# Performance work log

Measured on AMD Instinct MI355X. Metric: run time of the kernel, lower is better.

## Reference

```python
import jax, jax.numpy as jnp
import numpy as np

N = 8192
D = 512


def setup_inputs() -> dict:
    key = jax.random.key(0)
    k1, k2, k3, k4 = jax.random.split(key, 4)
    U = jax.random.normal(k1, (N, D), dtype=jnp.float32)
    V = jax.random.normal(k2, (N, D), dtype=jnp.float32)
    M = jax.random.normal(k3, (N, N), dtype=jnp.float32)
    W = jax.random.uniform(k4, (N, N), dtype=jnp.float32)
    alpha = jnp.ones((1,), dtype=jnp.float32) * 0.1
    return {"U": U, "V": V, "M": M, "W": W, "alpha": alpha}


def reference(U, V, M, W, alpha):
    # Reconstruction term: sum((U V^T - M)^2)
    recon = U @ V.T                                  # (N, N) GEMM
    part1 = jnp.sum(jnp.square(recon - M))
    # Manifold term in closed form:
    # sum_{i,j} W[i,j] * ||U_i - V_j||^2
    #   = sum_i rowW_i ||U_i||^2 + sum_j colW_j ||V_j||^2 - 2 sum(W * U V^T)
    u_sq = jnp.sum(U * U, axis=1)                    # (N,)
    v_sq = jnp.sum(V * V, axis=1)                    # (N,)
    row_w = jnp.sum(W, axis=1)                       # (N,)
    col_w = jnp.sum(W, axis=0)                       # (N,)
    cross = jnp.sum(W * recon)
    part2 = alpha[0] * (jnp.dot(row_w, u_sq) + jnp.dot(col_w, v_sq) - 2.0 * cross)
    total = part1 + part2
    return total / (M.shape[0] * M.shape[1])
```

## Files before the change

### kernel.cpp

```cpp
#include <hip/hip_runtime.h>
#include <hip/hip_bf16.h>
#include <stdint.h>

#define N_DIM 8192
#define D_DIM 512
#define BM 128
#define BN 128
#define BK 64

typedef __attribute__((ext_vector_type(8))) short bf16x8;
typedef __attribute__((ext_vector_type(4))) float f32x4;

__device__ __forceinline__ unsigned short f2bf(float f) {
    unsigned int x = __float_as_uint(f);
    x += 0x7fffu + ((x >> 16) & 1u);
    return (unsigned short)(x >> 16);
}

__global__ void __launch_bounds__(256) prep_kernel(
    const float* __restrict__ U, const float* __restrict__ V,
    unsigned short* __restrict__ Ub, unsigned short* __restrict__ Vb,
    float* __restrict__ usq, float* __restrict__ vsq)
{
    int row = blockIdx.x;
    const float* src;
    unsigned short* dst;
    float* sq;
    if (row < N_DIM) {
        src = U + (size_t)row * D_DIM;
        dst = Ub + (size_t)row * D_DIM;
        sq  = usq + row;
    } else {
        int r = row - N_DIM;
        src = V + (size_t)r * D_DIM;
        dst = Vb + (size_t)r * D_DIM;
        sq  = vsq + r;
    }
    int t = threadIdx.x;
    float2 v = *reinterpret_cast<const float2*>(src + 2 * t);
    float s = v.x * v.x + v.y * v.y;
    ushort2 b;
    b.x = f2bf(v.x);
    b.y = f2bf(v.y);
    *reinterpret_cast<ushort2*>(dst + 2 * t) = b;

    #pragma unroll
    for (int o = 32; o > 0; o >>= 1) s += __shfl_down(s, o, 64);
    __shared__ float red[4];
    if ((t & 63) == 0) red[t >> 6] = s;
    __syncthreads();
    if (t == 0) *sq = red[0] + red[1] + red[2] + red[3];
}

__global__ void __launch_bounds__(256, 4) fused_kernel(
    const unsigned short* __restrict__ Ub, const unsigned short* __restrict__ Vb,
    const float* __restrict__ Mg, const float* __restrict__ Wg,
    const float* __restrict__ usq, const float* __restrict__ vsq,
    double* __restrict__ acc)
{
    __shared__ alignas(16) char smem[BM * BK * 2 + BN * BK * 2];
    __shared__ float red1[4], red2[4];
    char* As = smem;
    char* Bs = smem + BM * BK * 2;
    float* recs = (float*)smem;

    const int t    = threadIdx.x;
    const int lane = t & 63;
    const int wave = t >> 6;
    const int wm   = wave >> 1;
    const int wn   = wave & 1;

    const int bid    = (blockIdx.x & 7) * 512 + (blockIdx.x >> 3);
    const int tile_m = bid >> 6;
    const int tile_n = bid & 63;
    const int row0   = tile_m * BM;
    const int col0   = tile_n * BN;

    const f32x4 zero = {0.f, 0.f, 0.f, 0.f};
    f32x4 acc_r[4][4];
    #pragma unroll
    for (int i = 0; i < 4; ++i)
        #pragma unroll
        for (int j = 0; j < 4; ++j)
            acc_r[i][j] = zero;

    auto As3 = (__attribute__((address_space(3))) char*)As;
    auto Bs3 = (__attribute__((address_space(3))) char*)Bs;

    for (int kt = 0; kt < D_DIM / BK; ++kt) {
        const int k0 = kt * BK;
        #pragma unroll
        for (int c = 0; c < 4; ++c) {
            int s   = c * 256 + t;
            int row = s >> 3;
            int kg  = s & 7;
            int kgs = kg ^ (row & 7);
            const unsigned short* ga = Ub + (size_t)(row0 + row) * D_DIM + k0 + kgs * 8;
            __builtin_amdgcn_global_load_lds(
                (const __attribute__((address_space(1))) void*)ga,
                (__attribute__((address_space(3))) void*)(As3 + s * 16), 16, 0, 0);
            const unsigned short* gb = Vb + (size_t)(col0 + row) * D_DIM + k0 + kgs * 8;
            __builtin_amdgcn_global_load_lds(
                (const __attribute__((address_space(1))) void*)gb,
                (__attribute__((address_space(3))) void*)(Bs3 + s * 16), 16, 0, 0);
        }
        __syncthreads();

        #pragma unroll
        for (int kc = 0; kc < 2; ++kc) {
            bf16x8 af[4], bfr[4];
            const int kgw = kc * 4 + (lane >> 4);
            #pragma unroll
            for (int i = 0; i < 4; ++i) {
                int ra   = wm * 64 + i * 16 + (lane & 15);
                int offa = ra * (BK * 2) + ((kgw ^ (ra & 7)) * 16);
                af[i] = *reinterpret_cast<const bf16x8*>(As + offa);
                int rb   = wn * 64 + i * 16 + (lane & 15);
                int offb = rb * (BK * 2) + ((kgw ^ (rb & 7)) * 16);
                bfr[i] = *reinterpret_cast<const bf16x8*>(Bs + offb);
            }
            #pragma unroll
            for (int i = 0; i < 4; ++i)
                #pragma unroll
                for (int j = 0; j < 4; ++j)
                    acc_r[i][j] = __builtin_amdgcn_mfma_f32_16x16x32_bf16(
                        af[i], bfr[j], acc_r[i][j], 0, 0, 0);
        }
        __syncthreads();
    }

    const int rloc = t >> 5;
    const int c4   = (t & 31) * 4;
    const f32x4 vs = *reinterpret_cast<const f32x4*>(vsq + col0 + c4);

    float s1 = 0.f, s2 = 0.f;

    #pragma unroll
    for (int h = 0; h < 2; ++h) {
        if (wm == h) {
            #pragma unroll
            for (int i = 0; i < 4; ++i)
                #pragma unroll
                for (int j = 0; j < 4; ++j)
                    #pragma unroll
                    for (int q = 0; q < 4; ++q)
                        recs[(i * 16 + (lane >> 4) * 4 + q) * 128 +
                             wn * 64 + j * 16 + (lane & 15)] = acc_r[i][j][q];
        }
        __syncthreads();

        const float* Mrow = Mg + (size_t)(row0 + h * 64) * N_DIM + col0 + c4;
        const float* Wrow = Wg + (size_t)(row0 + h * 64) * N_DIM + col0 + c4;

        #pragma unroll
        for (int kk = 0; kk < 2; ++kk) {
            f32x4 mv[4], wv[4];
            float usr[4];
            #pragma unroll
            for (int b = 0; b < 4; ++b) {
                int r = rloc + (kk * 4 + b) * 8;
                mv[b]  = *reinterpret_cast<const f32x4*>(Mrow + (size_t)r * N_DIM);
                wv[b]  = *reinterpret_cast<const f32x4*>(Wrow + (size_t)r * N_DIM);
                usr[b] = usq[row0 + h * 64 + r];
            }
            #pragma unroll
            for (int b = 0; b < 4; ++b) {
                int r = rloc + (kk * 4 + b) * 8;
                f32x4 rc = *reinterpret_cast<const f32x4*>(recs + r * 128 + c4);
                #pragma unroll
                for (int c = 0; c < 4; ++c) {
                    float d = rc[c] - mv[b][c];
                    s1 = fmaf(d, d, s1);
                    s2 = fmaf(wv[b][c], usr[b] + vs[c] - 2.f * rc[c], s2);
                }
            }
        }
        __syncthreads();
    }

    #pragma unroll
    for (int o = 32; o > 0; o >>= 1) {
        s1 += __shfl_down(s1, o, 64);
        s2 += __shfl_down(s2, o, 64);
    }
    if (lane == 0) { red1[wave] = s1; red2[wave] = s2; }
    __syncthreads();
    if (t == 0) {
        double a1 = (double)red1[0] + red1[1] + red1[2] + red1[3];
        double a2 = (double)red2[0] + red2[1] + red2[2] + red2[3];
        atomicAdd(acc, a1);
        atomicAdd(acc + 1, a2);
    }
}

__global__ void finalize_kernel(const double* __restrict__ acc,
                                const float* __restrict__ alpha,
                                float* __restrict__ out)
{
    double tot = acc[0] + (double)alpha[0] * acc[1];
    out[0] = (float)(tot / ((double)N_DIM * (double)N_DIM));
}

extern "C" void kernel_launch(void* const* d_in, const int* in_sizes, int n_in,
                              void* d_out, int out_size, void* d_ws, size_t ws_size,
                              hipStream_t stream) {
    const float* U     = (const float*)d_in[0];
    const float* V     = (const float*)d_in[1];
    const float* Mg    = (const float*)d_in[2];
    const float* Wg    = (const float*)d_in[3];
    const float* alpha = (const float*)d_in[4];

    char* ws = (char*)d_ws;
    unsigned short* Ub = (unsigned short*)ws;
    unsigned short* Vb = (unsigned short*)(ws + 8u * 1024 * 1024);
    float* usq = (float*)(ws + 16u * 1024 * 1024);
    float* vsq = (float*)(ws + 16u * 1024 * 1024 + 32u * 1024);
    double* acc = (double*)(ws + 16u * 1024 * 1024 + 64u * 1024);

    hipMemsetAsync(acc, 0, 2 * sizeof(double), stream);
    prep_kernel<<<2 * N_DIM, 256, 0, stream>>>(U, V, Ub, Vb, usq, vsq);
    fused_kernel<<<(N_DIM / BM) * (N_DIM / BN), 256, 0, stream>>>(
        Ub, Vb, Mg, Wg, usq, vsq, acc);
    finalize_kernel<<<1, 1, 0, stream>>>(acc, alpha, (float*)d_out);
}
```

Measured before the change: 202.4 us.

## Process two column tiles per block, overlapping epilogue with second GEMM

Each block now computes two adjacent 128x128 output tiles. The M/W epilogue of the first tile is interleaved into the MFMA k-loop of the second tile, so the streaming of the large M and W matrices overlaps with matrix-core work. The reconstruction tile moves into its own padded LDS buffer (stride 132) to reduce bank conflicts, and the swizzled block ordering is dropped. This doubles accumulator registers (launch bounds lowered to 2 blocks per SM) and halves the grid, which may reduce occupancy and latency hiding.

```diff
diff --git a/kernel.cpp b/kernel.cpp
--- a/kernel.cpp
+++ b/kernel.cpp
@@ -7,6 +7,7 @@
 #define BM 128
 #define BN 128
 #define BK 64
+#define RSTR 132
 
 typedef __attribute__((ext_vector_type(8))) short bf16x8;
 typedef __attribute__((ext_vector_type(4))) float f32x4;
@@ -52,17 +53,17 @@
     if (t == 0) *sq = red[0] + red[1] + red[2] + red[3];
 }
 
-__global__ void __launch_bounds__(256, 4) fused_kernel(
+__global__ void __launch_bounds__(256, 2) fused_kernel(
     const unsigned short* __restrict__ Ub, const unsigned short* __restrict__ Vb,
     const float* __restrict__ Mg, const float* __restrict__ Wg,
     const float* __restrict__ usq, const float* __restrict__ vsq,
     double* __restrict__ acc)
 {
     __shared__ alignas(16) char smem[BM * BK * 2 + BN * BK * 2];
+    __shared__ alignas(16) float recs[64 * RSTR];
     __shared__ float red1[4], red2[4];
     char* As = smem;
     char* Bs = smem + BM * BK * 2;
-    float* recs = (float*)smem;
 
     const int t    = threadIdx.x;
     const int lane = t & 63;
@@ -70,73 +71,58 @@
     const int wm   = wave >> 1;
     const int wn   = wave & 1;
 
-    const int bid    = (blockIdx.x & 7) * 512 + (blockIdx.x >> 3);
-    const int tile_m = bid >> 6;
-    const int tile_n = bid & 63;
+    const int bid    = blockIdx.x;
+    const int tile_m = bid >> 5;
+    const int pair   = bid & 31;
     const int row0   = tile_m * BM;
-    const int col0   = tile_n * BN;
-
-    const f32x4 zero = {0.f, 0.f, 0.f, 0.f};
-    f32x4 acc_r[4][4];
-    #pragma unroll
-    for (int i = 0; i < 4; ++i)
-        #pragma unroll
-        for (int j = 0; j < 4; ++j)
-            acc_r[i][j] = zero;
+    const int col0_0 = (pair * 2) * BN;
+    const int col0_1 = (pair * 2 + 1) * BN;
+
+    const int rloc = t >> 5;
+    const int c4   = (t & 31) * 4;
+
+    float s1 = 0.f, s2 = 0.f;
 
     auto As3 = (__attribute__((address_space(3))) char*)As;
     auto Bs3 = (__attribute__((address_space(3))) char*)Bs;
 
-    for (int kt = 0; kt < D_DIM / BK; ++kt) {
-        const int k0 = kt * BK;
+    auto stage = [&](const unsigned short* Ua, const unsigned short* Va, int k0) {
         #pragma unroll
         for (int c = 0; c < 4; ++c) {
             int s   = c * 256 + t;
             int row = s >> 3;
             int kg  = s & 7;
             int kgs = kg ^ (row & 7);
-            const unsigned short* ga = Ub + (size_t)(row0 + row) * D_DIM + k0 + kgs * 8;
             __builtin_amdgcn_global_load_lds(
-                (const __attribute__((address_space(1))) void*)ga,
+                (const __attribute__((address_space(1))) void*)(Ua + (size_t)row * D_DIM + k0 + kgs * 8),
                 (__attribute__((address_space(3))) void*)(As3 + s * 16), 16, 0, 0);
-            const unsigned short* gb = Vb + (size_t)(col0 + row) * D_DIM + k0 + kgs * 8;
             __builtin_amdgcn_global_load_lds(
-                (const __attribute__((address_space(1))) void*)gb,
+                (const __attribute__((address_space(1))) void*)(Va + (size_t)row * D_DIM + k0 + kgs * 8),
                 (__attribute__((address_space(3))) void*)(Bs3 + s * 16), 16, 0, 0);
         }
-        __syncthreads();
-
+    };
+
+    auto mma = [&](f32x4 (&a)[4][4]) {
         #pragma unroll
         for (int kc = 0; kc < 2; ++kc) {
             bf16x8 af[4], bfr[4];
             const int kgw = kc * 4 + (lane >> 4);
             #pragma unroll
             for (int i = 0; i < 4; ++i) {
-                int ra   = wm * 64 + i * 16 + (lane & 15);
-                int offa = ra * (BK * 2) + ((kgw ^ (ra & 7)) * 16);
-                af[i] = *reinterpret_cast<const bf16x8*>(As + offa);
-                int rb   = wn * 64 + i * 16 + (lane & 15);
-                int offb = rb * (BK * 2) + ((kgw ^ (rb & 7)) * 16);
-                bfr[i] = *reinterpret_cast<const bf16x8*>(Bs + offb);
+                int ra = wm * 64 + i * 16 + (lane & 15);
+                af[i]  = *reinterpret_cast<const bf16x8*>(As + ra * (BK * 2) + ((kgw ^ (ra & 7)) * 16));
+                int rb = wn * 64 + i * 16 + (lane & 15);
+                bfr[i] = *reinterpret_cast<const bf16x8*>(Bs + rb * (BK * 2) + ((kgw ^ (rb & 7)) * 16));
             }
             #pragma unroll
             for (int i = 0; i < 4; ++i)
                 #pragma unroll
                 for (int j = 0; j < 4; ++j)
-                    acc_r[i][j] = __builtin_amdgcn_mfma_f32_16x16x32_bf16(
-                        af[i], bfr[j], acc_r[i][j], 0, 0, 0);
-        }
-        __syncthreads();
-    }
-
-    const int rloc = t >> 5;
-    const int c4   = (t & 31) * 4;
-    const f32x4 vs = *reinterpret_cast<const f32x4*>(vsq + col0 + c4);
-
-    float s1 = 0.f, s2 = 0.f;
-
-    #pragma unroll
-    for (int h = 0; h < 2; ++h) {
+                    a[i][j] = __builtin_amdgcn_mfma_f32_16x16x32_bf16(af[i], bfr[j], a[i][j], 0, 0, 0);
+        }
+    };
+
+    auto dump_half = [&](f32x4 (&a)[4][4], int h) {
         if (wm == h) {
             #pragma unroll
             for (int i = 0; i < 4; ++i)
@@ -144,13 +130,83 @@
                 for (int j = 0; j < 4; ++j)
                     #pragma unroll
                     for (int q = 0; q < 4; ++q)
-                        recs[(i * 16 + (lane >> 4) * 4 + q) * 128 +
-                             wn * 64 + j * 16 + (lane & 15)] = acc_r[i][j][q];
-        }
+                        recs[(i * 16 + (lane >> 4) * 4 + q) * RSTR +
+                             wn * 64 + j * 16 + (lane & 15)] = a[i][j][q];
+        }
+    };
+
+    const f32x4 zero = {0.f, 0.f, 0.f, 0.f};
+    const unsigned short* Ua = Ub + (size_t)row0 * D_DIM;
+
+    f32x4 a0[4][4];
+    #pragma unroll
+    for (int i = 0; i < 4; ++i)
+        #pragma unroll
+        for (int j = 0; j < 4; ++j) a0[i][j] = zero;
+    {
+        const unsigned short* Va = Vb + (size_t)col0_0 * D_DIM;
+        for (int kt = 0; kt < D_DIM / BK; ++kt) {
+            stage(Ua, Va, kt * BK);
+            __syncthreads();
+            mma(a0);
+            __syncthreads();
+        }
+    }
+    dump_half(a0, 0);
+
+    f32x4 a1[4][4];
+    #pragma unroll
+    for (int i = 0; i < 4; ++i)
+        #pragma unroll
+        for (int j = 0; j < 4; ++j) a1[i][j] = zero;
+
+    const f32x4 vs0 = *reinterpret_cast<const f32x4*>(vsq + col0_0 + c4);
+    {
+        const unsigned short* Va = Vb + (size_t)col0_1 * D_DIM;
+        #pragma unroll
+        for (int kt = 0; kt < D_DIM / BK; ++kt) {
+            stage(Ua, Va, kt * BK);
+            if (kt == 4) dump_half(a0, 1);
+            __syncthreads();
+
+            const int h   = kt >> 2;
+            const int sp  = kt & 3;
+            const int r0c = rloc + (2 * sp) * 8;
+            const int r1c = r0c + 8;
+            const float* Mp = Mg + (size_t)(row0 + h * 64) * N_DIM + col0_0 + c4;
+            const float* Wp = Wg + (size_t)(row0 + h * 64) * N_DIM + col0_0 + c4;
+            f32x4 mv0 = *reinterpret_cast<const f32x4*>(Mp + (size_t)r0c * N_DIM);
+            f32x4 mv1 = *reinterpret_cast<const f32x4*>(Mp + (size_t)r1c * N_DIM);
+            f32x4 wv0 = *reinterpret_cast<const f32x4*>(Wp + (size_t)r0c * N_DIM);
+            f32x4 wv1 = *reinterpret_cast<const f32x4*>(Wp + (size_t)r1c * N_DIM);
+            float us0 = usq[row0 + h * 64 + r0c];
+            float us1 = usq[row0 + h * 64 + r1c];
+
+            mma(a1);
+
+            f32x4 rc0 = *reinterpret_cast<const f32x4*>(recs + r0c * RSTR + c4);
+            f32x4 rc1 = *reinterpret_cast<const f32x4*>(recs + r1c * RSTR + c4);
+            #pragma unroll
+            for (int c = 0; c < 4; ++c) {
+                float d0 = rc0[c] - mv0[c];
+                s1 = fmaf(d0, d0, s1);
+                s2 = fmaf(wv0[c], us0 + vs0[c] - 2.f * rc0[c], s2);
+                float d1 = rc1[c] - mv1[c];
+                s1 = fmaf(d1, d1, s1);
+                s2 = fmaf(wv1[c], us1 + vs0[c] - 2.f * rc1[c], s2);
+            }
+            __syncthreads();
+        }
+    }
+
+    const f32x4 vs1 = *reinterpret_cast<const f32x4*>(vsq + col0_1 + c4);
+    #pragma unroll
+    for (int hh = 0; hh < 2; ++hh) {
+        dump_half(a1, hh);
         __syncthreads();
 
-        const float* Mrow = Mg + (size_t)(row0 + h * 64) * N_DIM + col0 + c4;
-        const float* Wrow = Wg + (size_t)(row0 + h * 64) * N_DIM + col0 + c4;
+        const float* Mp = Mg + (size_t)(row0 + hh * 64) * N_DIM + col0_1 + c4;
+        const float* Wp = Wg + (size_t)(row0 + hh * 64) * N_DIM + col0_1 + c4;
 
         #pragma unroll
         for (int kk = 0; kk < 2; ++kk) {
@@ -158,20 +214,20 @@
             float usr[4];
             #pragma unroll
             for (int b = 0; b < 4; ++b) {
-                int r = rloc + (kk * 4 + b) * 8;
-                mv[b]  = *reinterpret_cast<const f32x4*>(Mrow + (size_t)r * N_DIM);
-                wv[b]  = *reinterpret_cast<const f32x4*>(Wrow + (size_t)r * N_DIM);
-                usr[b] = usq[row0 + h * 64 + r];
+                int r  = rloc + (kk * 4 + b) * 8;
+                mv[b]  = *reinterpret_cast<const f32x4*>(Mp + (size_t)r * N_DIM);
+                wv[b]  = *reinterpret_cast<const f32x4*>(Wp + (size_t)r * N_DIM);
+                usr[b] = usq[row0 + hh * 64 + r];
             }
             #pragma unroll
             for (int b = 0; b < 4; ++b) {
                 int r = rloc + (kk * 4 + b) * 8;
-                f32x4 rc = *reinterpret_cast<const f32x4*>(recs + r * 128 + c4);
+                f32x4 rc = *reinterpret_cast<const f32x4*>(recs + r * RSTR + c4);
                 #pragma unroll
                 for (int c = 0; c < 4; ++c) {
                     float d = rc[c] - mv[b][c];
                     s1 = fmaf(d, d, s1);
-                    s2 = fmaf(wv[b][c], usr[b] + vs[c] - 2.f * rc[c], s2);
+                    s2 = fmaf(wv[b][c], usr[b] + vs1[c] - 2.f * rc[c], s2);
                 }
             }
         }
@@ -186,10 +242,10 @@
     if (lane == 0) { red1[wave] = s1; red2[wave] = s2; }
     __syncthreads();
     if (t == 0) {
-        double a1 = (double)red1[0] + red1[1] + red1[2] + red1[3];
-        double a2 = (double)red2[0] + red2[1] + red2[2] + red2[3];
-        atomicAdd(acc, a1);
-        atomicAdd(acc + 1, a2);
+        double a1s = (double)red1[0] + red1[1] + red1[2] + red1[3];
+        double a2s = (double)red2[0] + red2[1] + red2[2] + red2[3];
+        atomicAdd(acc, a1s);
+        atomicAdd(acc + 1, a2s);
     }
 }
 
@@ -219,7 +275,7 @@
 
     hipMemsetAsync(acc, 0, 2 * sizeof(double), stream);
     prep_kernel<<<2 * N_DIM, 256, 0, stream>>>(U, V, Ub, Vb, usq, vsq);
-    fused_kernel<<<(N_DIM / BM) * (N_DIM / BN), 256, 0, stream>>>(
+    fused_kernel<<<(N_DIM / BM) * (N_DIM / BN) / 2, 256, 0, stream>>>(
         Ub, Vb, Mg, Wg, usq, vsq, acc);
     finalize_kernel<<<1, 1, 0, stream>>>(acc, alpha, (float*)d_out);
 }
```

After: 273.9 us. 35.3% more time.
